# Kernel tuning notes

Measured on AMD Instinct MI355X. Metric: run time of the kernel, lower is better.

## Reference

```python
import jax, jax.numpy as jnp
import numpy as np
from jax import lax

B, C, H, W = 4, 512, 64, 64
C8 = C // 8
OUT = 256
BN_EPS = 1e-5


def setup_inputs() -> dict:
    key = jax.random.key(0)
    ks = jax.random.split(key, 12)
    s = lambda k, shape, fan: jax.random.normal(k, shape, jnp.float32) * (1.0 / np.sqrt(fan))
    return {
        "x": jax.random.normal(ks[0], (B, C, H, W), jnp.float32),
        "wq": s(ks[1], (C8, C), C), "bq": jnp.zeros((C8,), jnp.float32),
        "wk": s(ks[2], (C8, C), C), "bk": jnp.zeros((C8,), jnp.float32),
        "wv": s(ks[3], (C, C), C),  "bv": jnp.zeros((C,), jnp.float32),
        "ca_w1": s(ks[4], (C8, C), C),
        "ca_w2": s(ks[5], (C, C8), C8),
        "conv_w": s(ks[6], (OUT, C, 3, 3), C * 9),
        "bn_gamma": jnp.ones((OUT,), jnp.float32),
        "bn_beta": jnp.zeros((OUT,), jnp.float32),
        "bn_mean": jnp.zeros((OUT,), jnp.float32),
        "bn_var": jnp.ones((OUT,), jnp.float32),
    }


def reference(x, wq, bq, wk, bk, wv, bv, ca_w1, ca_w2, conv_w,
              bn_gamma, bn_beta, bn_mean, bn_var):
    b, c, h, w = x.shape
    n = h * w
    xf = x.reshape(b, c, n)  # [B,C,N]

    # ---- Position attention ----
    q = jnp.einsum('qc,bcn->bnq', wq, xf) + bq            # [B,N,C8]
    k = jnp.einsum('kc,bcn->bkn', wk, xf) + bk[:, None]   # [B,C8,N]
    energy = jnp.einsum('bnq,bqm->bnm', q, k)             # [B,N,N]
    attn = jax.nn.softmax(energy, axis=-1)
    v = jnp.einsum('vc,bcn->bvn', wv, xf) + bv[:, None]   # [B,C,N]
    # torch: bmm(value, attention^T) -> out[b,c,m] = sum_n v[b,c,n]*attn[b,m,n]
    pa = jnp.einsum('bcn,bmn->bcm', v, attn).reshape(b, c, h, w) + x

    # ---- Channel attention (SE-style, avg+max pooled, shared MLP) ----
    avg = jnp.mean(pa, axis=(2, 3))   # [B,C]
    mx = jnp.max(pa, axis=(2, 3))     # [B,C]
    fc = lambda z: jnp.einsum('oc,bc->bo', ca_w2,
                              jax.nn.relu(jnp.einsum('hc,bc->bh', ca_w1, z)))
    scale = jax.nn.sigmoid(fc(avg) + fc(mx))[:, :, None, None]
    ca = scale * pa

    # ---- Conv 3x3 + BN (eval mode) + ReLU ----
    y = lax.conv_general_dilated(ca, conv_w, (1, 1), 'SAME',
                                 dimension_numbers=('NCHW', 'OIHW', 'NCHW'))
    inv = lax.rsqrt(bn_var + BN_EPS)
    y = (y - bn_mean[:, None, None]) * (inv * bn_gamma)[:, None, None] + bn_beta[:, None, None]
    return jax.nn.relu(y)
```

## Files before the change

kernel.cpp:

```cpp
#include <hip/hip_runtime.h>

#define NB 4
#define CIN 512
#define NPIX 4096
#define CQK 64
#define COUT 256
#define PPIX 4356

typedef __bf16 bh16;
typedef _Float16 fh16;
typedef __attribute__((ext_vector_type(8))) __bf16 bf16x8;
typedef __attribute__((ext_vector_type(8))) _Float16 f16x8;
typedef __attribute__((ext_vector_type(16))) float f32x16;

#define AS1 __attribute__((address_space(1)))
#define AS3 __attribute__((address_space(3)))

__device__ __forceinline__ void glds16(const void* g, void* l) {
  __builtin_amdgcn_global_load_lds((const AS1 unsigned int*)g, (AS3 unsigned int*)l, 16, 0, 0);
}

__device__ __forceinline__ float fexp2(float x) {
#if __has_builtin(__builtin_amdgcn_exp2f)
  return __builtin_amdgcn_exp2f(x);
#else
  return __expf(x * 0.6931471805599453f);
#endif
}

__global__ __launch_bounds__(256) void transpose_bf_k(const float* __restrict__ src,
                                                      bh16* __restrict__ dst) {
  __shared__ float tile[64][65];
  const int b = blockIdx.z;
  const int n0 = blockIdx.x * 64;
  const int c0 = blockIdx.y * 64;
  const float* s = src + (size_t)b * CIN * NPIX;
  bh16* d = dst + (size_t)b * CIN * NPIX;
  const int t = threadIdx.x;
  const int q4 = (t & 15) * 4;
  const int rr = t >> 4;
#pragma unroll
  for (int i = 0; i < 4; i++) {
    const int c = rr + i * 16;
    const float4 v = *(const float4*)&s[(size_t)(c0 + c) * NPIX + n0 + q4];
    tile[q4 + 0][c] = v.x;
    tile[q4 + 1][c] = v.y;
    tile[q4 + 2][c] = v.z;
    tile[q4 + 3][c] = v.w;
  }
  __syncthreads();
#pragma unroll
  for (int i = 0; i < 4; i++) {
    const int n = rr + i * 16;
    union { bh16 h[4]; ushort4 u; } pk;
    pk.h[0] = (bh16)tile[n][q4 + 0];
    pk.h[1] = (bh16)tile[n][q4 + 1];
    pk.h[2] = (bh16)tile[n][q4 + 2];
    pk.h[3] = (bh16)tile[n][q4 + 3];
    *(ushort4*)(void*)&d[(size_t)(n0 + n) * CIN + c0 + q4] = pk.u;
  }
}

__global__ __launch_bounds__(256) void wcast_k(const float* __restrict__ wq,
                                               const float* __restrict__ wk,
                                               const float* __restrict__ wv,
                                               const float* __restrict__ bq,
                                               const float* __restrict__ bk,
                                               bh16* __restrict__ Wqk,
                                               bh16* __restrict__ wvb,
                                               float* __restrict__ bias128) {
  const int idx = blockIdx.x * 256 + threadIdx.x;
  if (idx < 65536) {
    Wqk[idx] = (bh16)(idx < 32768 ? wq[idx] : wk[idx - 32768]);
  } else {
    const int j = idx - 65536;
    wvb[j] = (bh16)wv[j];
  }
  if (idx < 128) bias128[idx] = idx < 64 ? bq[idx] : bk[idx - 64];
}

__global__ __launch_bounds__(256) void qk_proj_k(const bh16* __restrict__ xTb,
                                                 const bh16* __restrict__ Wqk,
                                                 const float* __restrict__ bias128,
                                                 bh16* __restrict__ Qb,
                                                 bh16* __restrict__ Kf) {
  const int blk = blockIdx.x;
  const int t = threadIdx.x;
  const int w = t >> 6, l31 = t & 31, hi = (t & 63) >> 5;
  __shared__ __align__(16) bh16 As[2][64 * 64];
  f32x16 acc[2];
#pragma unroll
  for (int nt = 0; nt < 2; nt++)
#pragma unroll
    for (int r = 0; r < 16; r++) acc[nt][r] = 0.0f;

#define QK_STAGE(kc, buf)                                                           \
  {                                                                                 \
    _Pragma("unroll") for (int i = 0; i < 2; i++) {                                 \
      const int s = i * 256 + t;                                                    \
      const int n = s >> 3, slot = s & 7;                                           \
      glds16(xTb + (size_t)(blk * 64 + n) * CIN + (kc) * 64 + (((slot + n) & 7) * 8), \
             &As[buf][(size_t)(i * 256 + w * 64) * 8]);                             \
    }                                                                               \
  }

  QK_STAGE(0, 0);
  __syncthreads();
  for (int kc = 0; kc < 8; kc++) {
    if (kc < 7) QK_STAGE(kc + 1, (kc + 1) & 1);
    const bh16* as = As[kc & 1];
#pragma unroll
    for (int ks = 0; ks < 4; ks++) {
      const bf16x8 bfr = *(const bf16x8*)(Wqk + (size_t)(w * 32 + l31) * CIN + kc * 64 + ks * 16 + hi * 8);
      const int kk = ks * 2 + hi;
#pragma unroll
      for (int nt = 0; nt < 2; nt++) {
        const int n = nt * 32 + l31;
        const bf16x8 a = *(const bf16x8*)&as[(size_t)(n * 8 + ((kk - n) & 7)) * 8];
        acc[nt] = __builtin_amdgcn_mfma_f32_32x32x16_bf16(a, bfr, acc[nt], 0, 0, 0);
      }
    }
    __syncthreads();
  }
#undef QK_STAGE
  const int o = w * 32 + l31;
  const float bo = bias128[o];
  if (w < 2) {
#pragma unroll
    for (int nt = 0; nt < 2; nt++)
#pragma unroll
      for (int r = 0; r < 16; r++) {
        const int nloc = nt * 32 + (r & 3) + 8 * (r >> 2) + 4 * hi;
        Qb[(size_t)(blk * 64 + nloc) * 64 + o] = (bh16)((acc[nt][r] + bo) * 1.44269504088896f);
      }
  } else {
    const int b = blk >> 6, jtile = blk & 63;
    const int k = o - 64, kg = k >> 3, k7 = k & 7;
    bh16* kdst = Kf + (((size_t)(b * 64 + jtile) * 8 + kg) * 64) * 8 + k7;
#pragma unroll
    for (int nt = 0; nt < 2; nt++)
#pragma unroll
      for (int r = 0; r < 16; r++) {
        const int j = nt * 32 + (r & 3) + 8 * (r >> 2) + 4 * hi;
        kdst[(size_t)j * 8] = (bh16)(acc[nt][r] + bo);
      }
  }
}

__global__ __launch_bounds__(256) void v_proj_k(const bh16* __restrict__ xTb,
                                                const bh16* __restrict__ wvb,
                                                const float* __restrict__ bv,
                                                bh16* __restrict__ Vf) {
  const int nblk = blockIdx.x;
  const int cblk = blockIdx.y;
  const int b = blockIdx.z;
  const int t = threadIdx.x;
  const int w = t >> 6, l31 = t & 31, hi = (t & 63) >> 5;
  __shared__ __align__(16) bh16 Bs[2][256 * 64];
  f32x16 acc[2][2];
#pragma unroll
  for (int mt = 0; mt < 2; mt++)
#pragma unroll
    for (int nt = 0; nt < 2; nt++)
#pragma unroll
      for (int r = 0; r < 16; r++) acc[mt][nt][r] = 0.0f;

#define V_STAGE(kc, buf)                                                              \
  {                                                                                   \
    _Pragma("unroll") for (int i = 0; i < 8; i++) {                                   \
      const int s = i * 256 + t;                                                      \
      const int n = s >> 3, slot = s & 7;                                             \
      glds16(xTb + (size_t)(b * NPIX + nblk * 256 + n) * CIN + (kc) * 64 + (((slot + n) & 7) * 8), \
             &Bs[buf][(size_t)(i * 256 + w * 64) * 8]);                               \
    }                                                                                 \
  }

  V_STAGE(0, 0);
  __syncthreads();
  for (int kc = 0; kc < 8; kc++) {
    if (kc < 7) V_STAGE(kc + 1, (kc + 1) & 1);
    const bh16* bs = Bs[kc & 1];
#pragma unroll
    for (int ks = 0; ks < 4; ks++) {
      const int kk = ks * 2 + hi;
      bf16x8 a[2], bfr[2];
#pragma unroll
      for (int mt = 0; mt < 2; mt++)
        a[mt] = *(const bf16x8*)(wvb + (size_t)(cblk * 64 + mt * 32 + l31) * CIN + kc * 64 + ks * 16 + hi * 8);
#pragma unroll
      for (int nt = 0; nt < 2; nt++) {
        const int n = w * 64 + nt * 32 + l31;
        bfr[nt] = *(const bf16x8*)&bs[(size_t)(n * 8 + ((kk - n) & 7)) * 8];
      }
#pragma unroll
      for (int mt = 0; mt < 2; mt++)
#pragma unroll
        for (int nt = 0; nt < 2; nt++)
          acc[mt][nt] = __builtin_amdgcn_mfma_f32_32x32x16_bf16(a[mt], bfr[nt], acc[mt][nt], 0, 0, 0);
    }
    __syncthreads();
  }
#undef V_STAGE
  const int ntile0 = nblk * 4 + w;
#pragma unroll
  for (int mt = 0; mt < 2; mt++)
#pragma unroll
    for (int r = 0; r < 16; r++) {
      const int c = cblk * 64 + mt * 32 + (r & 3) + 8 * (r >> 2) + 4 * hi;
      const float bvc = bv[c];
#pragma unroll
      for (int nt = 0; nt < 2; nt++) {
        const int nl = nt * 32 + l31;
        Vf[(((size_t)(b * 64 + ntile0) * 8 + (nl >> 3)) * 512 + c) * 8 + (nl & 7)] =
            (bh16)(acc[mt][nt][r] + bvc);
      }
    }
}

__global__ __launch_bounds__(256, 2) void attn1p_k(const bh16* __restrict__ Qb,
                                                   const bh16* __restrict__ Kf,
                                                   const bh16* __restrict__ Vf,
                                                   const float* __restrict__ x,
                                                   fh16* __restrict__ pa,
                                                   float* __restrict__ psum,
                                                   float* __restrict__ pmax) {
  const int id = blockIdx.x + 2 * (blockIdx.y + 64 * blockIdx.z);
  const int b = (id & 7) >> 1;
  const int cblk = id & 1;
  const int mblk = (id >> 3) * 64;
  const int t = threadIdx.x;
  const int w = t >> 6, l31 = t & 31, hi = (t >> 5) & 1;
  const int jhalf = w & 1, mhalf = w >> 1;
  __shared__ __align__(16) bh16 Ps[2][8 * 64 * 8];
  __shared__ float lred[4][32];
  __shared__ float linvL[64];

  bf16x8 qf[4];
  {
    const bh16* qrow = Qb + (size_t)(b * NPIX + mblk + mhalf * 32 + l31) * 64;
#pragma unroll
    for (int ks = 0; ks < 4; ks++) qf[ks] = *(const bf16x8*)(qrow + ks * 16 + hi * 8);
  }
  const bh16* kfb = Kf + (size_t)b * (64 * 8 * 64 * 8);
  const bh16* vfb = Vf + (size_t)b * (64 * 8 * 512 * 8);
  const int cbase = cblk * 256 + w * 64;

#define KADDR(tile, ks) (kfb + (((size_t)(tile) * 8 + (ks) * 2 + hi) * 64 + jhalf * 32 + l31) * 8)
#define VADDR(tile, ks, ct) (vfb + (((size_t)(tile) * 8 + (ks) * 2 + hi) * 512 + cbase + (ct) * 32 + l31) * 8)

  f32x16 acc[2][2];
#pragma unroll
  for (int mt = 0; mt < 2; mt++)
#pragma unroll
    for (int ct = 0; ct < 2; ct++)
#pragma unroll
      for (int r = 0; r < 16; r++) acc[mt][ct][r] = 0.0f;
  float4 lsacc;
  lsacc.x = 0.0f; lsacc.y = 0.0f; lsacc.z = 0.0f; lsacc.w = 0.0f;

  bf16x8 kf_nxt[4];
  bf16x8 vf_use[4][2];
  f32x16 s1;
  {
    bf16x8 k0[4];
#pragma unroll
    for (int ks = 0; ks < 4; ks++) {
      k0[ks] = *(const bf16x8*)KADDR(0, ks);
#pragma unroll
      for (int ct = 0; ct < 2; ct++) vf_use[ks][ct] = *(const bf16x8*)VADDR(0, ks, ct);
    }
#pragma unroll
    for (int ks = 0; ks < 4; ks++) kf_nxt[ks] = *(const bf16x8*)KADDR(1, ks);
#pragma unroll
    for (int r = 0; r < 16; r++) s1[r] = 0.0f;
#pragma unroll
    for (int ks = 0; ks < 4; ks++)
      s1 = __builtin_amdgcn_mfma_f32_32x32x16_bf16(k0[ks], qf[ks], s1, 0, 0, 0);
  }

  for (int it = 0; it < 64; it++) {
    __builtin_amdgcn_s_setprio(1);
    f32x16 s1n;
#pragma unroll
    for (int r = 0; r < 16; r++) s1n[r] = 0.0f;
#pragma unroll
    for (int ks = 0; ks < 4; ks++)
      s1n = __builtin_amdgcn_mfma_f32_32x32x16_bf16(kf_nxt[ks], qf[ks], s1n, 0, 0, 0);
    {
      const int kt = (it + 2 < 64) ? it + 2 : 63;
#pragma unroll
      for (int ks = 0; ks < 4; ks++) kf_nxt[ks] = *(const bf16x8*)KADDR(kt, ks);
    }

    const bh16* ps = Ps[(it + 1) & 1];
    bh16* psw = Ps[it & 1];
    if (it) {
#pragma unroll
      for (int ks = 0; ks < 4; ks++) {
        bf16x8 pf0 = *(const bf16x8*)&ps[(size_t)((ks * 2 + hi) * 64 + l31) * 8];
        bf16x8 pf1 = *(const bf16x8*)&ps[(size_t)((ks * 2 + hi) * 64 + 32 + l31) * 8];
        acc[0][0] = __builtin_amdgcn_mfma_f32_32x32x16_bf16(pf0, vf_use[ks][0], acc[0][0], 0, 0, 0);
        acc[0][1] = __builtin_amdgcn_mfma_f32_32x32x16_bf16(pf0, vf_use[ks][1], acc[0][1], 0, 0, 0);
        {
          union { bh16 h[4]; uint2 u2; } pk;
#pragma unroll
          for (int q = 0; q < 4; q++) {
            const float p = fexp2(s1[ks * 4 + q]);
            lsacc[q] += p;
            pk.h[q] = (bh16)p;
          }
          *(uint2*)(void*)&psw[(size_t)((jhalf * 4 + ks) * 64 + mhalf * 32 + l31) * 8 + hi * 4] = pk.u2;
        }
        acc[1][0] = __builtin_amdgcn_mfma_f32_32x32x16_bf16(pf1, vf_use[ks][0], acc[1][0], 0, 0, 0);
        acc[1][1] = __builtin_amdgcn_mfma_f32_32x32x16_bf16(pf1, vf_use[ks][1], acc[1][1], 0, 0, 0);
        vf_use[ks][0] = *(const bf16x8*)VADDR(it, ks, 0);
        vf_use[ks][1] = *(const bf16x8*)VADDR(it, ks, 1);
      }
    } else {
#pragma unroll
      for (int g = 0; g < 4; g++) {
        union { bh16 h[4]; uint2 u2; } pk;
#pragma unroll
        for (int q = 0; q < 4; q++) {
          const float p = fexp2(s1[g * 4 + q]);
          lsacc[q] += p;
          pk.h[q] = (bh16)p;
        }
        *(uint2*)(void*)&psw[(size_t)((jhalf * 4 + g) * 64 + mhalf * 32 + l31) * 8 + hi * 4] = pk.u2;
      }
    }
    __builtin_amdgcn_s_setprio(0);
    __syncthreads();
    s1 = s1n;
  }
  {
    const bh16* ps = Ps[1];
#pragma unroll
    for (int ks = 0; ks < 4; ks++) {
      bf16x8 pf0 = *(const bf16x8*)&ps[(size_t)((ks * 2 + hi) * 64 + l31) * 8];
      bf16x8 pf1 = *(const bf16x8*)&ps[(size_t)((ks * 2 + hi) * 64 + 32 + l31) * 8];
      acc[0][0] = __builtin_amdgcn_mfma_f32_32x32x16_bf16(pf0, vf_use[ks][0], acc[0][0], 0, 0, 0);
      acc[0][1] = __builtin_amdgcn_mfma_f32_32x32x16_bf16(pf0, vf_use[ks][1], acc[0][1], 0, 0, 0);
      acc[1][0] = __builtin_amdgcn_mfma_f32_32x32x16_bf16(pf1, vf_use[ks][0], acc[1][0], 0, 0, 0);
      acc[1][1] = __builtin_amdgcn_mfma_f32_32x32x16_bf16(pf1, vf_use[ks][1], acc[1][1], 0, 0, 0);
    }
  }
#undef KADDR
#undef VADDR

  float lsum = (lsacc.x + lsacc.y) + (lsacc.z + lsacc.w);
  lsum += __shfl_xor(lsum, 32);
  if (hi == 0) lred[w][l31] = lsum;
  __syncthreads();
  if (t < 64) linvL[t] = 1.0f / (lred[(t >> 5) * 2][t & 31] + lred[(t >> 5) * 2 + 1][t & 31]);
  __syncthreads();

  float csum[2] = {0.0f, 0.0f};
  float cmax[2] = {-1e30f, -1e30f};
#pragma unroll
  for (int mt = 0; mt < 2; mt++) {
#pragma unroll
    for (int g = 0; g < 4; g++) {
      const int mloc = mt * 32 + g * 8 + hi * 4;
      const float4 lv = *(const float4*)&linvL[mloc];
#pragma unroll
      for (int ct = 0; ct < 2; ct++) {
        const int c = cbase + ct * 32 + l31;
        const float4 xv = *(const float4*)&x[(size_t)(b * CIN + c) * NPIX + mblk + mloc];
        float r0 = acc[mt][ct][g * 4 + 0] * lv.x + xv.x;
        float r1 = acc[mt][ct][g * 4 + 1] * lv.y + xv.y;
        float r2 = acc[mt][ct][g * 4 + 2] * lv.z + xv.z;
        float r3 = acc[mt][ct][g * 4 + 3] * lv.w + xv.w;
        csum[ct] += (r0 + r1) + (r2 + r3);
        cmax[ct] = fmaxf(cmax[ct], fmaxf(fmaxf(r0, r1), fmaxf(r2, r3)));
        fh16* pd = pa + ((size_t)(b * NPIX) + mblk + mloc) * CIN + c;
        pd[0 * CIN] = (fh16)r0;
        pd[1 * CIN] = (fh16)r1;
        pd[2 * CIN] = (fh16)r2;
        pd[3 * CIN] = (fh16)r3;
      }
    }
  }
#pragma unroll
  for (int ct = 0; ct < 2; ct++) {
    csum[ct] += __shfl_xor(csum[ct], 32);
    cmax[ct] = fmaxf(cmax[ct], __shfl_xor(cmax[ct], 32));
  }
  if (hi == 0) {
    const int mb = mblk >> 6;
#pragma unroll
    for (int ct = 0; ct < 2; ct++) {
      const int c = cbase + ct * 32 + l31;
      psum[((size_t)b * 64 + mb) * CIN + c] = csum[ct];
      pmax[((size_t)b * 64 + mb) * CIN + c] = cmax[ct];
    }
  }
}

__global__ __launch_bounds__(256) void mlp2_k(const float* __restrict__ psum,
                                              const float* __restrict__ pmax,
                                              const float* __restrict__ w1,
                                              const float* __restrict__ w2,
                                              float* __restrict__ scale) {
  const int b = blockIdx.x;
  const int t = threadIdx.x;
  __shared__ float avg_l[CIN], max_l[CIN], hbuf[128];
#pragma unroll
  for (int h = 0; h < 2; h++) {
    const int c = t + h * 256;
    float s = 0.0f, m = -1e30f;
#pragma unroll
    for (int k = 0; k < 64; k++) {
      s += psum[((size_t)b * 64 + k) * CIN + c];
      m = fmaxf(m, pmax[((size_t)b * 64 + k) * CIN + c]);
    }
    avg_l[c] = s * (1.0f / 4096.0f);
    max_l[c] = m;
  }
  __syncthreads();
  if (t < 128) {
    const float* src = (t < 64) ? avg_l : max_l;
    const int o = t & 63;
    float sacc = 0.0f;
    for (int c = 0; c < CIN; c += 4) {
      const float4 wv = *(const float4*)&w1[o * CIN + c];
      sacc += wv.x * src[c] + wv.y * src[c + 1] + wv.z * src[c + 2] + wv.w * src[c + 3];
    }
    hbuf[t] = fmaxf(sacc, 0.0f);
  }
  __syncthreads();
#pragma unroll
  for (int h = 0; h < 2; h++) {
    const int c = t + h * 256;
    float sacc = 0.0f;
#pragma unroll
    for (int k = 0; k < 64; k += 4) {
      const float4 wv = *(const float4*)&w2[c * 64 + k];
      sacc += wv.x * (hbuf[k] + hbuf[64 + k]) + wv.y * (hbuf[k + 1] + hbuf[64 + k + 1]) +
              wv.z * (hbuf[k + 2] + hbuf[64 + k + 2]) + wv.w * (hbuf[k + 3] + hbuf[64 + k + 3]);
    }
    scale[b * CIN + c] = 1.0f / (1.0f + __expf(-sacc));
  }
}

__global__ __launch_bounds__(256) void pack_k(const fh16* __restrict__ pa,
                                              const float* __restrict__ scl,
                                              fh16* __restrict__ pab) {
  const int b = blockIdx.y;
  const int n0 = blockIdx.x * 8;
  const int t = threadIdx.x;
  __shared__ float sc[CIN];
#pragma unroll
  for (int h = 0; h < 2; h++) sc[t + h * 256] = scl[b * CIN + t + h * 256];
  __syncthreads();
  const int c2 = t * 2;
  const float s0 = sc[c2], s1 = sc[c2 + 1];
#pragma unroll
  for (int j = 0; j < 8; j++) {
    const int n = n0 + j;
    const int pp = ((n >> 6) + 1) * 66 + (n & 63) + 1;
    union { fh16 h[2]; unsigned int u; } v, o;
    v.u = *(const unsigned int*)(pa + ((size_t)b * NPIX + n) * CIN + c2);
    o.h[0] = (fh16)((float)v.h[0] * s0);
    o.h[1] = (fh16)((float)v.h[1] * s1);
    *(unsigned int*)(void*)(pab + ((size_t)b * PPIX + pp) * CIN + c2) = o.u;
  }
}

__global__ __launch_bounds__(256) void bzero_k(fh16* __restrict__ pab) {
  const int t = threadIdx.x;
  const int p = blockIdx.x * 4 + (t >> 6);
  const int b = blockIdx.y;
  int pp;
  if (p < 66) pp = p;
  else if (p < 132) pp = 65 * 66 + (p - 66);
  else if (p < 196) pp = (p - 131) * 66;
  else pp = (p - 195) * 66 + 65;
  uint4 z = {0u, 0u, 0u, 0u};
  *(uint4*)(void*)(pab + ((size_t)b * PPIX + pp) * CIN + (t & 63) * 8) = z;
}

__global__ __launch_bounds__(256) void wpack_k(const float* __restrict__ cw,
                                               fh16* __restrict__ wp) {
  const int slot = blockIdx.x * 256 + threadIdx.x;
  const int oblk = slot / 36864;
  const int r1 = slot - oblk * 36864;
  const int chunk = r1 / 1152;
  const int r2 = r1 - chunk * 1152;
  const int tap = r2 >> 7;
  const int r3 = r2 & 127;
  const int h = r3 >> 6;
  const int o = r3 & 63;
  const size_t sbase = (size_t)(oblk * 64 + o) * 4608 + (size_t)(chunk * 16 + h * 8) * 9 + tap;
  union { fh16 h8[8]; uint4 u4; } pk;
#pragma unroll
  for (int i = 0; i < 8; i++) pk.h8[i] = (fh16)cw[sbase + (size_t)i * 9];
  *(uint4*)(void*)(wp + (size_t)slot * 8) = pk.u4;
}

__global__ __launch_bounds__(256) void conv_mfma_k(const fh16* __restrict__ pab,
                                                   const fh16* __restrict__ wp,
                                                   const float* __restrict__ gamma,
                                                   const float* __restrict__ beta,
                                                   const float* __restrict__ mean,
                                                   const float* __restrict__ var,
                                                   float* __restrict__ out) {
  const int y0 = blockIdx.x * 4;
  const int oblk = blockIdx.y;
  const int b = blockIdx.z;
  const int t = threadIdx.x;
  const int w = t >> 6, lane = t & 63, l31 = lane & 31, hi = lane >> 5;
  __shared__ __align__(16) fh16 Xs[2][416 * 16];
  __shared__ __align__(16) fh16 Ws[2][9 * 64 * 16];
  __shared__ float sb[64], bb[64];
  if (t < 64) {
    const int o = oblk * 64 + t;
    const float inv = rsqrtf(var[o] + 1e-5f);
    const float sc = inv * gamma[o];
    sb[t] = sc;
    bb[t] = beta[o] - mean[o] * sc;
  }
  f32x16 o00, o01, o10, o11;
#pragma unroll
  for (int r = 0; r < 16; r++) { o00[r] = 0.0f; o01[r] = 0.0f; o10[r] = 0.0f; o11[r] = 0.0f; }

  const fh16* xbase = pab + ((size_t)b * PPIX + y0 * 66) * CIN + (size_t)(lane & 31) * CIN + (lane >> 5) * 8;
  const fh16* wbase = wp + (size_t)oblk * 32 * 9216 + lane * 8;

#define STAGE(chunk, buf)                                                        \
  {                                                                              \
    const fh16* xs = xbase + (chunk) * 16;                                       \
    for (int i = w; i < 13; i += 4)                                              \
      glds16(xs + (size_t)i * 32 * CIN, &Xs[buf][i * 512]);                      \
    const fh16* wsrc = wbase + (size_t)(chunk) * 9216;                           \
    for (int i = w; i < 18; i += 4)                                              \
      glds16(wsrc + (size_t)i * 512, &Ws[buf][i * 512]);                         \
  }

  STAGE(0, 0);
  __syncthreads();
  for (int chunk = 0; chunk < 32; chunk++) {
    if (chunk < 31) STAGE(chunk + 1, (chunk + 1) & 1);
    const fh16* xs = Xs[chunk & 1];
    const fh16* ws = Ws[chunk & 1];
#pragma unroll
    for (int tap = 0; tap < 9; tap++) {
      const int ky = tap / 3, kx = tap - ky * 3;
      const f16x8 a0 = *(const f16x8*)&ws[tap * 1024 + hi * 512 + l31 * 8];
      const f16x8 a1 = *(const f16x8*)&ws[tap * 1024 + hi * 512 + (32 + l31) * 8];
      const int row0 = (w + ky) * 66 + l31 + kx;
      const int row1 = row0 + 32;
      const f16x8 b0 = *(const f16x8*)&xs[(row0 >> 5) * 512 + hi * 256 + (row0 & 31) * 8];
      const f16x8 b1 = *(const f16x8*)&xs[(row1 >> 5) * 512 + hi * 256 + (row1 & 31) * 8];
      o00 = __builtin_amdgcn_mfma_f32_32x32x16_f16(a0, b0, o00, 0, 0, 0);
      o01 = __builtin_amdgcn_mfma_f32_32x32x16_f16(a0, b1, o01, 0, 0, 0);
      o10 = __builtin_amdgcn_mfma_f32_32x32x16_f16(a1, b0, o10, 0, 0, 0);
      o11 = __builtin_amdgcn_mfma_f32_32x32x16_f16(a1, b1, o11, 0, 0, 0);
    }
    __syncthreads();
  }
#undef STAGE

  const f32x16* accs[2][2] = {{&o00, &o01}, {&o10, &o11}};
#pragma unroll
  for (int mt = 0; mt < 2; mt++) {
#pragma unroll
    for (int nt = 0; nt < 2; nt++) {
      const f32x16& A = *accs[mt][nt];
#pragma unroll
      for (int r = 0; r < 16; r++) {
        const int cl = mt * 32 + (r & 3) + 8 * (r >> 2) + 4 * hi;
        const int pix = nt * 32 + l31;
        const float y = A[r] * sb[cl] + bb[cl];
        out[((size_t)(b * COUT + oblk * 64 + cl)) * NPIX + (y0 + w) * 64 + pix] = fmaxf(y, 0.0f);
      }
    }
  }
}

extern "C" void kernel_launch(void* const* d_in, const int* in_sizes, int n_in,
                              void* d_out, int out_size, void* d_ws, size_t ws_size,
                              hipStream_t stream) {
  (void)in_sizes; (void)n_in; (void)out_size; (void)ws_size;
  const float* x        = (const float*)d_in[0];
  const float* wq       = (const float*)d_in[1];
  const float* bq       = (const float*)d_in[2];
  const float* wk       = (const float*)d_in[3];
  const float* bk       = (const float*)d_in[4];
  const float* wv       = (const float*)d_in[5];
  const float* bv       = (const float*)d_in[6];
  const float* ca_w1    = (const float*)d_in[7];
  const float* ca_w2    = (const float*)d_in[8];
  const float* conv_w   = (const float*)d_in[9];
  const float* bn_gamma = (const float*)d_in[10];
  const float* bn_beta  = (const float*)d_in[11];
  const float* bn_mean  = (const float*)d_in[12];
  const float* bn_var   = (const float*)d_in[13];
  float* out = (float*)d_out;

  float* ws = (float*)d_ws;
  fh16*  pa      = (fh16*)ws;
  float* psum    = ws + 4194304;
  float* pmax    = ws + 4325376;
  bh16*  Vf      = (bh16*)(ws + 8388608);
  fh16*  wpck    = (fh16*)(ws + 8388608);
  bh16*  Qb      = (bh16*)(ws + 12582912);
  bh16*  Kf      = (bh16*)(ws + 13107200);
  bh16*  xTb     = (bh16*)(ws + 13631488);
  fh16*  pab     = (fh16*)(ws + 13631488);
  bh16*  Wqk     = (bh16*)(ws + 17825792);
  bh16*  wvb     = (bh16*)(ws + 17858560);
  float* bias128 = ws + 17989632;
  float* scl     = ws + 18104320;

  wcast_k<<<dim3(1280, 1, 1), 256, 0, stream>>>(wq, wk, wv, bq, bk, Wqk, wvb, bias128);
  transpose_bf_k<<<dim3(NPIX / 64, CIN / 64, NB), 256, 0, stream>>>(x, xTb);
  qk_proj_k<<<dim3(256, 1, 1), 256, 0, stream>>>(xTb, Wqk, bias128, Qb, Kf);
  v_proj_k<<<dim3(16, 8, NB), 256, 0, stream>>>(xTb, wvb, bv, Vf);
  attn1p_k<<<dim3(2, 64, NB), 256, 0, stream>>>(Qb, Kf, Vf, x, pa, psum, pmax);
  bzero_k<<<dim3(65, NB, 1), 256, 0, stream>>>(pab);
  mlp2_k<<<dim3(NB, 1, 1), 256, 0, stream>>>(psum, pmax, ca_w1, ca_w2, scl);
  pack_k<<<dim3(NPIX / 8, NB, 1), 256, 0, stream>>>(pa, scl, pab);
  wpack_k<<<dim3(576, 1, 1), 256, 0, stream>>>(conv_w, wpck);
  conv_mfma_k<<<dim3(16, 4, NB), 256, 0, stream>>>(pab, wpck, bn_gamma, bn_beta,
                                                   bn_mean, bn_var, out);
}
```

Measured before the change: 328.7 us.

## Halve conv output-channel tile, split MLP dot products, and lighten attention barriers

The conv kernel now handles 32 output channels per block instead of 64, which doubles the grid to 512 blocks and halves the weight staging and accumulators. This raises parallelism at the cost of more reloads of the input tile. The attention loop drops the setprio calls and replaces __syncthreads with a custom lgkmcnt wait plus s_barrier. It also removes the clamp on the K prefetch index, so the final iterations read past the last K tile. The MLP's first layer now splits each dot product across two threads and combines them with a shuffle, so all 256 threads take part.

```diff
diff --git a/kernel.cpp b/kernel.cpp
--- a/kernel.cpp
+++ b/kernel.cpp
@@ -18,6 +18,10 @@
 
 __device__ __forceinline__ void glds16(const void* g, void* l) {
   __builtin_amdgcn_global_load_lds((const AS1 unsigned int*)g, (AS3 unsigned int*)l, 16, 0, 0);
+}
+
+__device__ __forceinline__ void lbar() {
+  asm volatile("s_waitcnt lgkmcnt(0)\n\ts_barrier" ::: "memory");
 }
 
 __device__ __forceinline__ float fexp2(float x) {
@@ -279,7 +283,6 @@
   }
 
   for (int it = 0; it < 64; it++) {
-    __builtin_amdgcn_s_setprio(1);
     f32x16 s1n;
 #pragma unroll
     for (int r = 0; r < 16; r++) s1n[r] = 0.0f;
@@ -287,9 +290,8 @@
     for (int ks = 0; ks < 4; ks++)
       s1n = __builtin_amdgcn_mfma_f32_32x32x16_bf16(kf_nxt[ks], qf[ks], s1n, 0, 0, 0);
     {
-      const int kt = (it + 2 < 64) ? it + 2 : 63;
-#pragma unroll
-      for (int ks = 0; ks < 4; ks++) kf_nxt[ks] = *(const bf16x8*)KADDR(kt, ks);
+#pragma unroll
+      for (int ks = 0; ks < 4; ks++) kf_nxt[ks] = *(const bf16x8*)KADDR(it + 2, ks);
     }
 
     const bh16* ps = Ps[(it + 1) & 1];
@@ -329,8 +331,7 @@
         *(uint2*)(void*)&psw[(size_t)((jhalf * 4 + g) * 64 + mhalf * 32 + l31) * 8 + hi * 4] = pk.u2;
       }
     }
-    __builtin_amdgcn_s_setprio(0);
-    __syncthreads();
+    lbar();
     s1 = s1n;
   }
   {
@@ -418,15 +419,19 @@
     max_l[c] = m;
   }
   __syncthreads();
-  if (t < 128) {
-    const float* src = (t < 64) ? avg_l : max_l;
-    const int o = t & 63;
+  {
+    const int d = t >> 1;
+    const int hf = t & 1;
+    const float* src = (d < 64) ? avg_l : max_l;
+    const int o = d & 63;
     float sacc = 0.0f;
-    for (int c = 0; c < CIN; c += 4) {
+    const int c0 = hf * 256;
+    for (int c = c0; c < c0 + 256; c += 4) {
       const float4 wv = *(const float4*)&w1[o * CIN + c];
       sacc += wv.x * src[c] + wv.y * src[c + 1] + wv.z * src[c + 2] + wv.w * src[c + 3];
     }
-    hbuf[t] = fmaxf(sacc, 0.0f);
+    sacc += __shfl_xor(sacc, 1);
+    if (hf == 0) hbuf[d] = fmaxf(sacc, 0.0f);
   }
   __syncthreads();
 #pragma unroll
@@ -483,15 +488,15 @@
 __global__ __launch_bounds__(256) void wpack_k(const float* __restrict__ cw,
                                                fh16* __restrict__ wp) {
   const int slot = blockIdx.x * 256 + threadIdx.x;
-  const int oblk = slot / 36864;
-  const int r1 = slot - oblk * 36864;
-  const int chunk = r1 / 1152;
-  const int r2 = r1 - chunk * 1152;
-  const int tap = r2 >> 7;
-  const int r3 = r2 & 127;
-  const int h = r3 >> 6;
-  const int o = r3 & 63;
-  const size_t sbase = (size_t)(oblk * 64 + o) * 4608 + (size_t)(chunk * 16 + h * 8) * 9 + tap;
+  const int oblk = slot / 18432;
+  const int r1 = slot - oblk * 18432;
+  const int chunk = r1 / 576;
+  const int r2 = r1 - chunk * 576;
+  const int tap = r2 >> 6;
+  const int r3 = r2 & 63;
+  const int h = r3 >> 5;
+  const int o = r3 & 31;
+  const size_t sbase = (size_t)(oblk * 32 + o) * 4608 + (size_t)(chunk * 16 + h * 8) * 9 + tap;
   union { fh16 h8[8]; uint4 u4; } pk;
 #pragma unroll
   for (int i = 0; i < 8; i++) pk.h8[i] = (fh16)cw[sbase + (size_t)i * 9];
@@ -511,29 +516,29 @@
   const int t = threadIdx.x;
   const int w = t >> 6, lane = t & 63, l31 = lane & 31, hi = lane >> 5;
   __shared__ __align__(16) fh16 Xs[2][416 * 16];
-  __shared__ __align__(16) fh16 Ws[2][9 * 64 * 16];
-  __shared__ float sb[64], bb[64];
-  if (t < 64) {
-    const int o = oblk * 64 + t;
+  __shared__ __align__(16) fh16 Ws[2][9 * 2 * 32 * 8];
+  __shared__ float sb[32], bb[32];
+  if (t < 32) {
+    const int o = oblk * 32 + t;
     const float inv = rsqrtf(var[o] + 1e-5f);
     const float sc = inv * gamma[o];
     sb[t] = sc;
     bb[t] = beta[o] - mean[o] * sc;
   }
-  f32x16 o00, o01, o10, o11;
-#pragma unroll
-  for (int r = 0; r < 16; r++) { o00[r] = 0.0f; o01[r] = 0.0f; o10[r] = 0.0f; o11[r] = 0.0f; }
-
-  const fh16* xbase = pab + ((size_t)b * PPIX + y0 * 66) * CIN + (size_t)(lane & 31) * CIN + (lane >> 5) * 8;
-  const fh16* wbase = wp + (size_t)oblk * 32 * 9216 + lane * 8;
+  f32x16 o00, o01;
+#pragma unroll
+  for (int r = 0; r < 16; r++) { o00[r] = 0.0f; o01[r] = 0.0f; }
+
+  const fh16* xbase = pab + ((size_t)b * PPIX + y0 * 66) * CIN + (size_t)l31 * CIN + hi * 8;
+  const fh16* wbase = wp + (size_t)oblk * 147456 + lane * 8;
 
 #define STAGE(chunk, buf)                                                        \
   {                                                                              \
     const fh16* xs = xbase + (chunk) * 16;                                       \
     for (int i = w; i < 13; i += 4)                                              \
       glds16(xs + (size_t)i * 32 * CIN, &Xs[buf][i * 512]);                      \
-    const fh16* wsrc = wbase + (size_t)(chunk) * 9216;                           \
-    for (int i = w; i < 18; i += 4)                                              \
+    const fh16* wsrc = wbase + (size_t)(chunk) * 4608;                           \
+    for (int i = w; i < 9; i += 4)                                               \
       glds16(wsrc + (size_t)i * 512, &Ws[buf][i * 512]);                         \
   }
 
@@ -546,34 +551,28 @@
 #pragma unroll
     for (int tap = 0; tap < 9; tap++) {
       const int ky = tap / 3, kx = tap - ky * 3;
-      const f16x8 a0 = *(const f16x8*)&ws[tap * 1024 + hi * 512 + l31 * 8];
-      const f16x8 a1 = *(const f16x8*)&ws[tap * 1024 + hi * 512 + (32 + l31) * 8];
+      const f16x8 a0 = *(const f16x8*)&ws[tap * 512 + hi * 256 + l31 * 8];
       const int row0 = (w + ky) * 66 + l31 + kx;
       const int row1 = row0 + 32;
       const f16x8 b0 = *(const f16x8*)&xs[(row0 >> 5) * 512 + hi * 256 + (row0 & 31) * 8];
       const f16x8 b1 = *(const f16x8*)&xs[(row1 >> 5) * 512 + hi * 256 + (row1 & 31) * 8];
       o00 = __builtin_amdgcn_mfma_f32_32x32x16_f16(a0, b0, o00, 0, 0, 0);
       o01 = __builtin_amdgcn_mfma_f32_32x32x16_f16(a0, b1, o01, 0, 0, 0);
-      o10 = __builtin_amdgcn_mfma_f32_32x32x16_f16(a1, b0, o10, 0, 0, 0);
-      o11 = __builtin_amdgcn_mfma_f32_32x32x16_f16(a1, b1, o11, 0, 0, 0);
     }
     __syncthreads();
   }
 #undef STAGE
 
-  const f32x16* accs[2][2] = {{&o00, &o01}, {&o10, &o11}};
-#pragma unroll
-  for (int mt = 0; mt < 2; mt++) {
-#pragma unroll
-    for (int nt = 0; nt < 2; nt++) {
-      const f32x16& A = *accs[mt][nt];
-#pragma unroll
-      for (int r = 0; r < 16; r++) {
-        const int cl = mt * 32 + (r & 3) + 8 * (r >> 2) + 4 * hi;
-        const int pix = nt * 32 + l31;
-        const float y = A[r] * sb[cl] + bb[cl];
-        out[((size_t)(b * COUT + oblk * 64 + cl)) * NPIX + (y0 + w) * 64 + pix] = fmaxf(y, 0.0f);
-      }
+  const f32x16* accs[2] = {&o00, &o01};
+#pragma unroll
+  for (int nt = 0; nt < 2; nt++) {
+    const f32x16& A = *accs[nt];
+#pragma unroll
+    for (int r = 0; r < 16; r++) {
+      const int cl = (r & 3) + 8 * (r >> 2) + 4 * hi;
+      const int pix = nt * 32 + l31;
+      const float y = A[r] * sb[cl] + bb[cl];
+      out[((size_t)(b * COUT + oblk * 32 + cl)) * NPIX + (y0 + w) * 64 + pix] = fmaxf(y, 0.0f);
     }
   }
 }
@@ -622,6 +621,6 @@
   mlp2_k<<<dim3(NB, 1, 1), 256, 0, stream>>>(psum, pmax, ca_w1, ca_w2, scl);
   pack_k<<<dim3(NPIX / 8, NB, 1), 256, 0, stream>>>(pa, scl, pab);
   wpack_k<<<dim3(576, 1, 1), 256, 0, stream>>>(conv_w, wpck);
-  conv_mfma_k<<<dim3(16, 4, NB), 256, 0, stream>>>(pab, wpck, bn_gamma, bn_beta,
+  conv_mfma_k<<<dim3(16, 8, NB), 256, 0, stream>>>(pab, wpck, bn_gamma, bn_beta,
                                                    bn_mean, bn_var, out);
 }
```

Measured after the change: 318.4 us. 1.03x faster.
